# Kernel optimization log

Hardware: AMD Instinct MI355X
Metric: run time of the kernel (lower is better)

Reference implementation:

```python
import jax, jax.numpy as jnp
import numpy as np

N_NODES = 100000
N_EDGES = 1600000
IN_DIM = 128
HID_DIM = 64
OUT_DIM = 128
EPS = 1e-5


def setup_inputs() -> dict:
    key = jax.random.key(0)
    ks = jax.random.split(key, 10)
    feat = jax.random.normal(ks[0], (N_NODES, IN_DIM), dtype=jnp.float32)
    src = jax.random.randint(ks[1], (N_EDGES,), 0, N_NODES)
    dst = jax.random.randint(ks[2], (N_EDGES,), 0, N_NODES)
    # learned params
    gamma = jnp.ones((IN_DIM,), jnp.float32)
    beta = jnp.zeros((IN_DIM,), jnp.float32)
    Wq = jax.random.normal(ks[3], (IN_DIM, HID_DIM), jnp.float32) * 0.05
    bq = jax.random.normal(ks[4], (HID_DIM,), jnp.float32) * 0.05
    Wk = jax.random.normal(ks[5], (IN_DIM, HID_DIM), jnp.float32) * 0.05
    Wv = jax.random.normal(ks[6], (IN_DIM, OUT_DIM), jnp.float32) * 0.05
    We = jax.random.normal(ks[7], (HID_DIM, 1), jnp.float32) * 0.05
    return {"feat": feat, "src": src, "dst": dst, "gamma": gamma, "beta": beta,
            "Wq": Wq, "bq": bq, "Wk": Wk, "Wv": Wv, "We": We}


def reference(feat, src, dst, gamma, beta, Wq, bq, Wk, Wv, We):
    # BatchNorm1d (training-mode batch stats, biased variance)
    mean = jnp.mean(feat, axis=0)
    var = jnp.mean((feat - mean) ** 2, axis=0)
    x = (feat - mean) * jax.lax.rsqrt(var + EPS) * gamma + beta
    # feat_drop = 0.0 -> identity
    q = x @ Wq + bq          # [N, H]
    k = x @ Wk               # [N, H]
    v = x @ Wv               # [N, O]
    # u_add_v: src-node q + dst-node k per edge, then sigmoid and fc_e -> scalar score
    e = jax.nn.sigmoid(q[src] + k[dst]) @ We  # [E, 1]
    e = e[:, 0]                               # [E]
    # edge_softmax: softmax over incoming edges of each destination node
    m = jax.ops.segment_max(e, dst, num_segments=N_NODES)  # [N]
    ex = jnp.exp(e - m[dst])
    s = jax.ops.segment_sum(ex, dst, num_segments=N_NODES)  # [N]
    a = ex / s[dst]                                          # [E]
    # u_mul_e_sum: weighted scatter-sum of source v into destinations
    rst = jax.ops.segment_sum(v[src] * a[:, None], dst, num_segments=N_NODES)  # [N, O]
    return rst
```

## Files before the change

### kernel.cpp

```cpp
#include <hip/hip_runtime.h>
#include <math.h>

#define IN_DIM 128
#define HID 64
#define OUT_DIM 128
#define ELL_W 64
#define FA 512
#define FB 512
constexpr float EPS = 1e-5f;

typedef short short8 __attribute__((ext_vector_type(8)));
typedef float f32x4  __attribute__((ext_vector_type(4)));
typedef int   i32x4  __attribute__((ext_vector_type(4)));


__device__ inline ushort f2bf(float x) {
    __bf16 h = (__bf16)x;
    return *reinterpret_cast<ushort*>(&h);
}
__device__ inline short f2bfs(float x) {
    __bf16 h = (__bf16)x;
    return *reinterpret_cast<short*>(&h);
}
__device__ inline float bf2f(ushort u) {
    union { unsigned u; float f; } c; c.u = ((unsigned)u) << 16;
    return c.f;
}
__device__ inline float4 bf4_to_f4(ushort4 u) {
    return make_float4(bf2f(u.x), bf2f(u.y), bf2f(u.z), bf2f(u.w));
}

__device__ __forceinline__ void fill_edges(
    const int* __restrict__ src, const int* __restrict__ dst,
    int* __restrict__ deg, int* __restrict__ ell,
    int e0, int e1, int bid, int nblk)
{
    int idx    = bid * 256 + threadIdx.x;
    int stride = nblk * 256;
    int nv     = (e1 - e0) >> 2;
    const i32x4* d4p = reinterpret_cast<const i32x4*>(dst + e0);
    const i32x4* s4p = reinterpret_cast<const i32x4*>(src + e0);

    for (int i = idx; i < nv; i += stride) {
        i32x4 d4 = __builtin_nontemporal_load(d4p + i);
        i32x4 s4 = __builtin_nontemporal_load(s4p + i);
        #pragma unroll
        for (int j = 0; j < 4; j++) {
            int d = d4[j];
            int pos = atomicAdd(&deg[d], 1);
            if (pos < ELL_W) ell[(size_t)d * ELL_W + pos] = s4[j];
        }
    }
    for (int e = e0 + (nv << 2) + idx; e < e1; e += stride) {
        int d = dst[e];
        int pos = atomicAdd(&deg[d], 1);
        if (pos < ELL_W) ell[(size_t)d * ELL_W + pos] = src[e];
    }
}

__global__ __launch_bounds__(256) void preA(
    const float* __restrict__ feat, float* __restrict__ ws, int n_nodes,
    const float* __restrict__ Wq, const float* __restrict__ Wk,
    const float* __restrict__ Wv, ushort* __restrict__ Bfrag,
    const int* __restrict__ src, const int* __restrict__ dst,
    int* __restrict__ deg, int* __restrict__ ell, int e1)
{
    int t = threadIdx.x;
    if (blockIdx.x < 256) {
        __shared__ float redS[256], redQ[256];
        int col  = t & 127;
        int half = t >> 7;
        float sum = 0.f, sq = 0.f;
        for (int r = blockIdx.x * 2 + half; r < n_nodes; r += 512) {
            float x = feat[r * IN_DIM + col];
            sum += x; sq += x * x;
        }
        redS[t] = sum; redQ[t] = sq;
        __syncthreads();
        if (t < 128) {
            sum = redS[t] + redS[t + 128];
            sq  = redQ[t] + redQ[t + 128];
            unsafeAtomicAdd(&ws[col], sum);
            unsafeAtomicAdd(&ws[128 + col], sq);
        }
    } else if (blockIdx.x < 256 + 16) {
        int gid  = (blockIdx.x - 256) * 256 + t;
        int f    = gid >> 6;
        int lane = gid & 63;
        int kc = f & 3, ct = (f >> 2) & 3, w = f >> 4;
        int col   = w * 64 + ct * 16 + (lane & 15);
        int kbase = kc * 32 + (lane >> 4) * 8;
        ushort tmp[8];
        #pragma unroll
        for (int j = 0; j < 8; j++) {
            int k = kbase + j;
            float val;
            if (col < 64)       val = Wq[k * HID + col];
            else if (col < 128) val = Wk[k * HID + (col - 64)];
            else                val = Wv[k * OUT_DIM + (col - 128)];
            tmp[j] = f2bf(val);
        }
        ushort* d = &Bfrag[(f * 64 + lane) * 8];
        *(ushort4*)d       = make_ushort4(tmp[0], tmp[1], tmp[2], tmp[3]);
        *(ushort4*)(d + 4) = make_ushort4(tmp[4], tmp[5], tmp[6], tmp[7]);
    } else {
        fill_edges(src, dst, deg, ell, 0, e1, blockIdx.x - 272, FA);
    }
}

__global__ __launch_bounds__(256) void fusedB(
    const float* __restrict__ feat, const ushort* __restrict__ Bfrag,
    const float* __restrict__ bq,
    const float* __restrict__ gamma, const float* __restrict__ beta,
    const float* __restrict__ stats,
    ushort* __restrict__ qvb, ushort* __restrict__ kb, int n_nodes,
    const int* __restrict__ src, const int* __restrict__ dst,
    int* __restrict__ deg, int* __restrict__ ell, int e1, int n_edges,
    int mb)
{
    if (blockIdx.x >= mb) {
        fill_edges(src, dst, deg, ell, e1, n_edges, blockIdx.x - mb, FB);
        return;
    }

    __shared__ float sc[IN_DIM], sh[IN_DIM];
    int tid = threadIdx.x;
    if (tid < 128) {
        float inv_n = 1.0f / (float)n_nodes;
        float mean = stats[tid] * inv_n;
        float var  = stats[128 + tid] * inv_n - mean * mean;
        float s    = gamma[tid] * rsqrtf(var + EPS);
        sc[tid] = s; sh[tid] = beta[tid] - mean * s;
    }

    int w    = tid >> 6;
    int lane = tid & 63;
    int row0 = blockIdx.x * 64;
    int m    = lane & 15;
    int quad = lane >> 4;
    int nm1  = n_nodes - 1;

    short8 bfr[16];
    #pragma unroll
    for (int f = 0; f < 16; f++)
        bfr[f] = *(const short8*)&Bfrag[((w * 16 + f) * 64 + lane) * 8];

    __syncthreads();

    f32x4 acc[4][4] = {};

    #pragma unroll
    for (int kc = 0; kc < 4; kc++) {
        int koff = kc * 32 + quad * 8;
        float4 sc0 = *(const float4*)&sc[koff];
        float4 sc1 = *(const float4*)&sc[koff + 4];
        float4 sh0 = *(const float4*)&sh[koff];
        float4 sh1 = *(const float4*)&sh[koff + 4];
        short8 afr[4];
        #pragma unroll
        for (int rt = 0; rt < 4; rt++) {
            int row = row0 + rt * 16 + m;
            row = row < nm1 ? row : nm1;
            const float* fp = &feat[(size_t)row * IN_DIM + koff];
            float4 x0 = *(const float4*)fp;
            float4 x1 = *(const float4*)(fp + 4);
            afr[rt][0] = f2bfs(x0.x * sc0.x + sh0.x);
            afr[rt][1] = f2bfs(x0.y * sc0.y + sh0.y);
            afr[rt][2] = f2bfs(x0.z * sc0.z + sh0.z);
            afr[rt][3] = f2bfs(x0.w * sc0.w + sh0.w);
            afr[rt][4] = f2bfs(x1.x * sc1.x + sh1.x);
            afr[rt][5] = f2bfs(x1.y * sc1.y + sh1.y);
            afr[rt][6] = f2bfs(x1.z * sc1.z + sh1.z);
            afr[rt][7] = f2bfs(x1.w * sc1.w + sh1.w);
        }
        #pragma unroll
        for (int rt = 0; rt < 4; rt++)
            #pragma unroll
            for (int ct = 0; ct < 4; ct++)
                acc[rt][ct] = __builtin_amdgcn_mfma_f32_16x16x32_bf16(
                    afr[rt], bfr[ct * 4 + kc], acc[rt][ct], 0, 0, 0);
    }

    ushort* base; int ld, cl;
    if (w == 1)      { base = kb;  ld = HID; cl = 0; }
    else             { base = qvb; ld = 192; cl = (w == 0) ? 0 : 64 * (w - 1); }

    #pragma unroll
    for (int ct = 0; ct < 4; ct++) {
        int col = cl + ct * 16 + m;
        float bias = (w == 0) ? bq[ct * 16 + m] : 0.f;
        #pragma unroll
        for (int rt = 0; rt < 4; rt++) {
            int r0 = row0 + rt * 16 + quad * 4;
            #pragma unroll
            for (int r = 0; r < 4; r++)
                base[(size_t)(r0 + r) * ld + col] = f2bf(acc[rt][ct][r] + bias);
        }
    }
}

__global__ __launch_bounds__(256) void gather_ell(
    const int* __restrict__ deg, const int* __restrict__ ell,
    const ushort* __restrict__ qvb, const ushort* __restrict__ kb,
    const float* __restrict__ We,
    float* __restrict__ out, int n_nodes)
{
    int node = (blockIdx.x * 256 + threadIdx.x) >> 6;
    int lane = threadIdx.x & 63;
    if (node >= n_nodes) return;
    int h   = lane & 15;
    int sub = lane >> 4;
    int cnt = deg[node];
    cnt = cnt < ELL_W ? cnt : ELL_W;

    if (cnt == 0) {
        if (sub == 0) {
            float4 z = make_float4(0.f, 0.f, 0.f, 0.f);
            *(float4*)&out[node * OUT_DIM + 4 * h]      = z;
            *(float4*)&out[node * OUT_DIM + 64 + 4 * h] = z;
        }
        return;
    }

    const int* row = &ell[(size_t)node * ELL_W];
    float4 kd = bf4_to_f4(*(const ushort4*)&kb[node * HID + 4 * h]);
    float4 we = *(const float4*)&We[4 * h];
    const float L2E = 1.4426950408889634f;
    we.x *= L2E; we.y *= L2E; we.z *= L2E; we.w *= L2E;

    float4 o0 = make_float4(0.f, 0.f, 0.f, 0.f);
    float4 o1 = make_float4(0.f, 0.f, 0.f, 0.f);
    float ssum = 0.f;

    for (int p0 = 0; p0 < cnt; p0 += 4) {
        int p = p0 + sub;
        bool act = (p < cnt);
        int sN = row[act ? p : 0];
        const ushort* qv = qvb + (size_t)sN * 192;
        float4 qq = bf4_to_f4(*(const ushort4*)(qv + 4 * h));
        float t;
        t  = we.x * __fdividef(1.f, 1.f + __expf(-(qq.x + kd.x)));
        t += we.y * __fdividef(1.f, 1.f + __expf(-(qq.y + kd.y)));
        t += we.z * __fdividef(1.f, 1.f + __expf(-(qq.z + kd.z)));
        t += we.w * __fdividef(1.f, 1.f + __expf(-(qq.w + kd.w)));
        t += __shfl_xor(t, 1);
        t += __shfl_xor(t, 2);
        t += __shfl_xor(t, 4);
        t += __shfl_xor(t, 8);
        float exv = act ? exp2f(t) : 0.f;
        ssum += exv;
        float4 v0 = bf4_to_f4(*(const ushort4*)(qv + 64 + 4 * h));
        float4 v1 = bf4_to_f4(*(const ushort4*)(qv + 128 + 4 * h));
        o0.x += exv * v0.x; o0.y += exv * v0.y;
        o0.z += exv * v0.z; o0.w += exv * v0.w;
        o1.x += exv * v1.x; o1.y += exv * v1.y;
        o1.z += exv * v1.z; o1.w += exv * v1.w;
    }

    ssum += __shfl_xor(ssum, 16); ssum += __shfl_xor(ssum, 32);
    o0.x += __shfl_xor(o0.x, 16); o0.x += __shfl_xor(o0.x, 32);
    o0.y += __shfl_xor(o0.y, 16); o0.y += __shfl_xor(o0.y, 32);
    o0.z += __shfl_xor(o0.z, 16); o0.z += __shfl_xor(o0.z, 32);
    o0.w += __shfl_xor(o0.w, 16); o0.w += __shfl_xor(o0.w, 32);
    o1.x += __shfl_xor(o1.x, 16); o1.x += __shfl_xor(o1.x, 32);
    o1.y += __shfl_xor(o1.y, 16); o1.y += __shfl_xor(o1.y, 32);
    o1.z += __shfl_xor(o1.z, 16); o1.z += __shfl_xor(o1.z, 32);
    o1.w += __shfl_xor(o1.w, 16); o1.w += __shfl_xor(o1.w, 32);

    if (sub == 0) {
        float inv = (ssum > 0.f) ? __fdividef(1.f, ssum) : 0.f;
        o0.x *= inv; o0.y *= inv; o0.z *= inv; o0.w *= inv;
        o1.x *= inv; o1.y *= inv; o1.z *= inv; o1.w *= inv;
        *(float4*)&out[node * OUT_DIM + 4 * h]      = o0;
        *(float4*)&out[node * OUT_DIM + 64 + 4 * h] = o1;
    }
}

extern "C" void kernel_launch(void* const* d_in, const int* in_sizes, int n_in,
                              void* d_out, int out_size, void* d_ws, size_t ws_size,
                              hipStream_t stream)
{
    const float* feat  = (const float*)d_in[0];
    const int*   src   = (const int*)d_in[1];
    const int*   dst   = (const int*)d_in[2];
    const float* gamma = (const float*)d_in[3];
    const float* beta  = (const float*)d_in[4];
    const float* Wq    = (const float*)d_in[5];
    const float* bq    = (const float*)d_in[6];
    const float* Wk    = (const float*)d_in[7];
    const float* Wv    = (const float*)d_in[8];
    const float* We    = (const float*)d_in[9];

    int n_nodes = in_sizes[0] / IN_DIM;
    int n_edges = in_sizes[1];
    int n_pad   = n_nodes + 64;
    int mb      = (n_nodes + 63) / 64;
    int e1      = ((n_edges * 9) / 20) & ~3;

    float* ws = (float*)d_ws;

    int* deg = (int*)(ws + 256);
    int* ell = deg + n_nodes;
    size_t off = 256 + (size_t)n_nodes * (1 + ELL_W);
    off = (off + 3) & ~(size_t)3;
    ushort* qvb   = (ushort*)(ws + off);
    ushort* kb    = qvb + (size_t)n_pad * 192;
    ushort* Bfrag = kb + (size_t)n_pad * HID;

    hipMemsetAsync(ws, 0, (256 + (size_t)n_nodes) * sizeof(float), stream);
    preA<<<256 + 16 + FA, 256, 0, stream>>>(
        feat, ws, n_nodes, Wq, Wk, Wv, Bfrag, src, dst, deg, ell, e1);
    fusedB<<<mb + FB, 256, 0, stream>>>(
        feat, Bfrag, bq, gamma, beta, ws, qvb, kb, n_nodes,
        src, dst, deg, ell, e1, n_edges, mb);
    long long g_threads = (long long)n_nodes * 64;
    gather_ell<<<(int)((g_threads + 255) / 256), 256, 0, stream>>>(
        deg, ell, qvb, kb, We, (float*)d_out, n_nodes);
}
```

Baseline: 409.5 us.

## Fuse all stages into one persistent cooperative kernel with grid syncs

Replaces the memset plus three launches with a single cooperative persistent kernel. It zeroes the workspace, builds the weight fragments, computes BatchNorm stats, fills the ELL adjacency, runs the MFMA projections and does the edge-softmax gather, with grid-wide syncs between phases. This removes launch overhead and the memset. In exchange it serializes edge filling after the stats pass, where before that work overlapped with other stages. It also drops the vectorized nontemporal edge loads and adds grid-sync costs, with persistent loops over nodes replacing a full grid for the gather.

```diff
diff --git a/kernel.cpp b/kernel.cpp
--- a/kernel.cpp
+++ b/kernel.cpp
@@ -1,17 +1,17 @@
 #include <hip/hip_runtime.h>
+#include <hip/hip_cooperative_groups.h>
 #include <math.h>
+
+namespace cg = cooperative_groups;
 
 #define IN_DIM 128
 #define HID 64
 #define OUT_DIM 128
 #define ELL_W 64
-#define FA 512
-#define FB 512
 constexpr float EPS = 1e-5f;
 
 typedef short short8 __attribute__((ext_vector_type(8)));
 typedef float f32x4  __attribute__((ext_vector_type(4)));
-typedef int   i32x4  __attribute__((ext_vector_type(4)));
 
 
 __device__ inline ushort f2bf(float x) {
@@ -30,66 +30,36 @@
     return make_float4(bf2f(u.x), bf2f(u.y), bf2f(u.z), bf2f(u.w));
 }
 
-__device__ __forceinline__ void fill_edges(
+__global__ __launch_bounds__(256, 4) void mega(
+    const float* __restrict__ feat,
     const int* __restrict__ src, const int* __restrict__ dst,
-    int* __restrict__ deg, int* __restrict__ ell,
-    int e0, int e1, int bid, int nblk)
+    const float* __restrict__ gamma, const float* __restrict__ beta,
+    const float* __restrict__ Wq, const float* __restrict__ bq,
+    const float* __restrict__ Wk, const float* __restrict__ Wv,
+    const float* __restrict__ We,
+    float* __restrict__ ws, int* __restrict__ deg, int* __restrict__ ell,
+    ushort* __restrict__ qvb, ushort* __restrict__ kb,
+    ushort* __restrict__ Bfrag, float* __restrict__ out,
+    int n_nodes, int n_edges, int mb)
 {
-    int idx    = bid * 256 + threadIdx.x;
-    int stride = nblk * 256;
-    int nv     = (e1 - e0) >> 2;
-    const i32x4* d4p = reinterpret_cast<const i32x4*>(dst + e0);
-    const i32x4* s4p = reinterpret_cast<const i32x4*>(src + e0);
-
-    for (int i = idx; i < nv; i += stride) {
-        i32x4 d4 = __builtin_nontemporal_load(d4p + i);
-        i32x4 s4 = __builtin_nontemporal_load(s4p + i);
-        #pragma unroll
-        for (int j = 0; j < 4; j++) {
-            int d = d4[j];
-            int pos = atomicAdd(&deg[d], 1);
-            if (pos < ELL_W) ell[(size_t)d * ELL_W + pos] = s4[j];
-        }
-    }
-    for (int e = e0 + (nv << 2) + idx; e < e1; e += stride) {
-        int d = dst[e];
-        int pos = atomicAdd(&deg[d], 1);
-        if (pos < ELL_W) ell[(size_t)d * ELL_W + pos] = src[e];
-    }
-}
-
-__global__ __launch_bounds__(256) void preA(
-    const float* __restrict__ feat, float* __restrict__ ws, int n_nodes,
-    const float* __restrict__ Wq, const float* __restrict__ Wk,
-    const float* __restrict__ Wv, ushort* __restrict__ Bfrag,
-    const int* __restrict__ src, const int* __restrict__ dst,
-    int* __restrict__ deg, int* __restrict__ ell, int e1)
-{
-    int t = threadIdx.x;
-    if (blockIdx.x < 256) {
-        __shared__ float redS[256], redQ[256];
-        int col  = t & 127;
-        int half = t >> 7;
-        float sum = 0.f, sq = 0.f;
-        for (int r = blockIdx.x * 2 + half; r < n_nodes; r += 512) {
-            float x = feat[r * IN_DIM + col];
-            sum += x; sq += x * x;
-        }
-        redS[t] = sum; redQ[t] = sq;
-        __syncthreads();
-        if (t < 128) {
-            sum = redS[t] + redS[t + 128];
-            sq  = redQ[t] + redQ[t + 128];
-            unsafeAtomicAdd(&ws[col], sum);
-            unsafeAtomicAdd(&ws[128 + col], sq);
-        }
-    } else if (blockIdx.x < 256 + 16) {
-        int gid  = (blockIdx.x - 256) * 256 + t;
+    cg::grid_group gg = cg::this_grid();
+    __shared__ float smem[512];
+    int t    = threadIdx.x;
+    int G    = (int)gridDim.x;
+    int gtid = (int)blockIdx.x * 256 + t;
+    int gsz  = G * 256;
+    int w    = t >> 6;
+    int lane = t & 63;
+
+    for (int i = gtid; i < 256; i += gsz) ws[i] = 0.f;
+    for (int i = gtid; i < n_nodes; i += gsz) deg[i] = 0;
+    if (blockIdx.x < 16) {
+        int gid  = (int)blockIdx.x * 256 + t;
         int f    = gid >> 6;
-        int lane = gid & 63;
-        int kc = f & 3, ct = (f >> 2) & 3, w = f >> 4;
-        int col   = w * 64 + ct * 16 + (lane & 15);
-        int kbase = kc * 32 + (lane >> 4) * 8;
+        int l    = gid & 63;
+        int kc = f & 3, ct = (f >> 2) & 3, ww = f >> 4;
+        int col   = ww * 64 + ct * 16 + (l & 15);
+        int kbase = kc * 32 + (l >> 4) * 8;
         ushort tmp[8];
         #pragma unroll
         for (int j = 0; j < 8; j++) {
@@ -100,179 +70,184 @@
             else                val = Wv[k * OUT_DIM + (col - 128)];
             tmp[j] = f2bf(val);
         }
-        ushort* d = &Bfrag[(f * 64 + lane) * 8];
+        ushort* d = &Bfrag[(f * 64 + l) * 8];
         *(ushort4*)d       = make_ushort4(tmp[0], tmp[1], tmp[2], tmp[3]);
         *(ushort4*)(d + 4) = make_ushort4(tmp[4], tmp[5], tmp[6], tmp[7]);
-    } else {
-        fill_edges(src, dst, deg, ell, 0, e1, blockIdx.x - 272, FA);
-    }
-}
-
-__global__ __launch_bounds__(256) void fusedB(
-    const float* __restrict__ feat, const ushort* __restrict__ Bfrag,
-    const float* __restrict__ bq,
-    const float* __restrict__ gamma, const float* __restrict__ beta,
-    const float* __restrict__ stats,
-    ushort* __restrict__ qvb, ushort* __restrict__ kb, int n_nodes,
-    const int* __restrict__ src, const int* __restrict__ dst,
-    int* __restrict__ deg, int* __restrict__ ell, int e1, int n_edges,
-    int mb)
-{
-    if (blockIdx.x >= mb) {
-        fill_edges(src, dst, deg, ell, e1, n_edges, blockIdx.x - mb, FB);
-        return;
-    }
-
-    __shared__ float sc[IN_DIM], sh[IN_DIM];
-    int tid = threadIdx.x;
-    if (tid < 128) {
-        float inv_n = 1.0f / (float)n_nodes;
-        float mean = stats[tid] * inv_n;
-        float var  = stats[128 + tid] * inv_n - mean * mean;
-        float s    = gamma[tid] * rsqrtf(var + EPS);
-        sc[tid] = s; sh[tid] = beta[tid] - mean * s;
-    }
-
-    int w    = tid >> 6;
-    int lane = tid & 63;
-    int row0 = blockIdx.x * 64;
-    int m    = lane & 15;
-    int quad = lane >> 4;
-    int nm1  = n_nodes - 1;
-
-    short8 bfr[16];
-    #pragma unroll
-    for (int f = 0; f < 16; f++)
-        bfr[f] = *(const short8*)&Bfrag[((w * 16 + f) * 64 + lane) * 8];
-
-    __syncthreads();
-
-    f32x4 acc[4][4] = {};
-
-    #pragma unroll
-    for (int kc = 0; kc < 4; kc++) {
-        int koff = kc * 32 + quad * 8;
-        float4 sc0 = *(const float4*)&sc[koff];
-        float4 sc1 = *(const float4*)&sc[koff + 4];
-        float4 sh0 = *(const float4*)&sh[koff];
-        float4 sh1 = *(const float4*)&sh[koff + 4];
-        short8 afr[4];
+    }
+    gg.sync();
+
+    {
+        int col  = t & 127;
+        int half = t >> 7;
+        float sum = 0.f, sq = 0.f;
+        for (int r = (int)blockIdx.x * 2 + half; r < n_nodes; r += G * 2) {
+            float x = feat[r * IN_DIM + col];
+            sum += x; sq += x * x;
+        }
+        smem[t] = sum; smem[256 + t] = sq;
+        __syncthreads();
+        if (t < 128) {
+            sum = smem[t] + smem[t + 128];
+            sq  = smem[256 + t] + smem[256 + t + 128];
+            unsafeAtomicAdd(&ws[t], sum);
+            unsafeAtomicAdd(&ws[128 + t], sq);
+        }
+    }
+    gg.sync();
+
+    for (int e = gtid; e < n_edges; e += gsz) {
+        int d = dst[e];
+        int s = src[e];
+        int pos = atomicAdd(&deg[d], 1);
+        if (pos < ELL_W) ell[(size_t)d * ELL_W + pos] = s;
+    }
+    gg.sync();
+
+    {
+        if (t < 128) {
+            float inv_n = 1.0f / (float)n_nodes;
+            float mean = ws[t] * inv_n;
+            float var  = ws[128 + t] * inv_n - mean * mean;
+            float s    = gamma[t] * rsqrtf(var + EPS);
+            smem[t] = s; smem[128 + t] = beta[t] - mean * s;
+        }
+        int m    = lane & 15;
+        int quad = lane >> 4;
+        int nm1  = n_nodes - 1;
+        short8 bfr[16];
         #pragma unroll
-        for (int rt = 0; rt < 4; rt++) {
-            int row = row0 + rt * 16 + m;
-            row = row < nm1 ? row : nm1;
-            const float* fp = &feat[(size_t)row * IN_DIM + koff];
-            float4 x0 = *(const float4*)fp;
-            float4 x1 = *(const float4*)(fp + 4);
-            afr[rt][0] = f2bfs(x0.x * sc0.x + sh0.x);
-            afr[rt][1] = f2bfs(x0.y * sc0.y + sh0.y);
-            afr[rt][2] = f2bfs(x0.z * sc0.z + sh0.z);
-            afr[rt][3] = f2bfs(x0.w * sc0.w + sh0.w);
-            afr[rt][4] = f2bfs(x1.x * sc1.x + sh1.x);
-            afr[rt][5] = f2bfs(x1.y * sc1.y + sh1.y);
-            afr[rt][6] = f2bfs(x1.z * sc1.z + sh1.z);
-            afr[rt][7] = f2bfs(x1.w * sc1.w + sh1.w);
-        }
-        #pragma unroll
-        for (int rt = 0; rt < 4; rt++)
+        for (int f = 0; f < 16; f++)
+            bfr[f] = *(const short8*)&Bfrag[((w * 16 + f) * 64 + lane) * 8];
+        __syncthreads();
+        const float* sc = smem;
+        const float* sh = smem + 128;
+
+        for (int mi = (int)blockIdx.x; mi < mb; mi += G) {
+            int row0 = mi * 64;
+            f32x4 acc[4][4] = {};
             #pragma unroll
-            for (int ct = 0; ct < 4; ct++)
-                acc[rt][ct] = __builtin_amdgcn_mfma_f32_16x16x32_bf16(
-                    afr[rt], bfr[ct * 4 + kc], acc[rt][ct], 0, 0, 0);
-    }
-
-    ushort* base; int ld, cl;
-    if (w == 1)      { base = kb;  ld = HID; cl = 0; }
-    else             { base = qvb; ld = 192; cl = (w == 0) ? 0 : 64 * (w - 1); }
-
-    #pragma unroll
-    for (int ct = 0; ct < 4; ct++) {
-        int col = cl + ct * 16 + m;
-        float bias = (w == 0) ? bq[ct * 16 + m] : 0.f;
-        #pragma unroll
-        for (int rt = 0; rt < 4; rt++) {
-            int r0 = row0 + rt * 16 + quad * 4;
+            for (int kc = 0; kc < 4; kc++) {
+                int koff = kc * 32 + quad * 8;
+                float4 sc0 = *(const float4*)&sc[koff];
+                float4 sc1 = *(const float4*)&sc[koff + 4];
+                float4 sh0 = *(const float4*)&sh[koff];
+                float4 sh1 = *(const float4*)&sh[koff + 4];
+                short8 afr[4];
+                #pragma unroll
+                for (int rt = 0; rt < 4; rt++) {
+                    int row = row0 + rt * 16 + m;
+                    row = row < nm1 ? row : nm1;
+                    const float* fp = &feat[(size_t)row * IN_DIM + koff];
+                    float4 x0 = *(const float4*)fp;
+                    float4 x1 = *(const float4*)(fp + 4);
+                    afr[rt][0] = f2bfs(x0.x * sc0.x + sh0.x);
+                    afr[rt][1] = f2bfs(x0.y * sc0.y + sh0.y);
+                    afr[rt][2] = f2bfs(x0.z * sc0.z + sh0.z);
+                    afr[rt][3] = f2bfs(x0.w * sc0.w + sh0.w);
+                    afr[rt][4] = f2bfs(x1.x * sc1.x + sh1.x);
+                    afr[rt][5] = f2bfs(x1.y * sc1.y + sh1.y);
+                    afr[rt][6] = f2bfs(x1.z * sc1.z + sh1.z);
+                    afr[rt][7] = f2bfs(x1.w * sc1.w + sh1.w);
+                }
+                #pragma unroll
+                for (int rt = 0; rt < 4; rt++)
+                    #pragma unroll
+                    for (int ct = 0; ct < 4; ct++)
+                        acc[rt][ct] = __builtin_amdgcn_mfma_f32_16x16x32_bf16(
+                            afr[rt], bfr[ct * 4 + kc], acc[rt][ct], 0, 0, 0);
+            }
+
+            ushort* base; int ld, cl;
+            if (w == 1)      { base = kb;  ld = HID; cl = 0; }
+            else             { base = qvb; ld = 192; cl = (w == 0) ? 0 : 64 * (w - 1); }
+
             #pragma unroll
-            for (int r = 0; r < 4; r++)
-                base[(size_t)(r0 + r) * ld + col] = f2bf(acc[rt][ct][r] + bias);
-        }
-    }
-}
-
-__global__ __launch_bounds__(256) void gather_ell(
-    const int* __restrict__ deg, const int* __restrict__ ell,
-    const ushort* __restrict__ qvb, const ushort* __restrict__ kb,
-    const float* __restrict__ We,
-    float* __restrict__ out, int n_nodes)
-{
-    int node = (blockIdx.x * 256 + threadIdx.x) >> 6;
-    int lane = threadIdx.x & 63;
-    if (node >= n_nodes) return;
-    int h   = lane & 15;
-    int sub = lane >> 4;
-    int cnt = deg[node];
-    cnt = cnt < ELL_W ? cnt : ELL_W;
-
-    if (cnt == 0) {
-        if (sub == 0) {
-            float4 z = make_float4(0.f, 0.f, 0.f, 0.f);
-            *(float4*)&out[node * OUT_DIM + 4 * h]      = z;
-            *(float4*)&out[node * OUT_DIM + 64 + 4 * h] = z;
-        }
-        return;
-    }
-
-    const int* row = &ell[(size_t)node * ELL_W];
-    float4 kd = bf4_to_f4(*(const ushort4*)&kb[node * HID + 4 * h]);
-    float4 we = *(const float4*)&We[4 * h];
-    const float L2E = 1.4426950408889634f;
-    we.x *= L2E; we.y *= L2E; we.z *= L2E; we.w *= L2E;
-
-    float4 o0 = make_float4(0.f, 0.f, 0.f, 0.f);
-    float4 o1 = make_float4(0.f, 0.f, 0.f, 0.f);
-    float ssum = 0.f;
-
-    for (int p0 = 0; p0 < cnt; p0 += 4) {
-        int p = p0 + sub;
-        bool act = (p < cnt);
-        int sN = row[act ? p : 0];
-        const ushort* qv = qvb + (size_t)sN * 192;
-        float4 qq = bf4_to_f4(*(const ushort4*)(qv + 4 * h));
-        float t;
-        t  = we.x * __fdividef(1.f, 1.f + __expf(-(qq.x + kd.x)));
-        t += we.y * __fdividef(1.f, 1.f + __expf(-(qq.y + kd.y)));
-        t += we.z * __fdividef(1.f, 1.f + __expf(-(qq.z + kd.z)));
-        t += we.w * __fdividef(1.f, 1.f + __expf(-(qq.w + kd.w)));
-        t += __shfl_xor(t, 1);
-        t += __shfl_xor(t, 2);
-        t += __shfl_xor(t, 4);
-        t += __shfl_xor(t, 8);
-        float exv = act ? exp2f(t) : 0.f;
-        ssum += exv;
-        float4 v0 = bf4_to_f4(*(const ushort4*)(qv + 64 + 4 * h));
-        float4 v1 = bf4_to_f4(*(const ushort4*)(qv + 128 + 4 * h));
-        o0.x += exv * v0.x; o0.y += exv * v0.y;
-        o0.z += exv * v0.z; o0.w += exv * v0.w;
-        o1.x += exv * v1.x; o1.y += exv * v1.y;
-        o1.z += exv * v1.z; o1.w += exv * v1.w;
-    }
-
-    ssum += __shfl_xor(ssum, 16); ssum += __shfl_xor(ssum, 32);
-    o0.x += __shfl_xor(o0.x, 16); o0.x += __shfl_xor(o0.x, 32);
-    o0.y += __shfl_xor(o0.y, 16); o0.y += __shfl_xor(o0.y, 32);
-    o0.z += __shfl_xor(o0.z, 16); o0.z += __shfl_xor(o0.z, 32);
-    o0.w += __shfl_xor(o0.w, 16); o0.w += __shfl_xor(o0.w, 32);
-    o1.x += __shfl_xor(o1.x, 16); o1.x += __shfl_xor(o1.x, 32);
-    o1.y += __shfl_xor(o1.y, 16); o1.y += __shfl_xor(o1.y, 32);
-    o1.z += __shfl_xor(o1.z, 16); o1.z += __shfl_xor(o1.z, 32);
-    o1.w += __shfl_xor(o1.w, 16); o1.w += __shfl_xor(o1.w, 32);
-
-    if (sub == 0) {
-        float inv = (ssum > 0.f) ? __fdividef(1.f, ssum) : 0.f;
-        o0.x *= inv; o0.y *= inv; o0.z *= inv; o0.w *= inv;
-        o1.x *= inv; o1.y *= inv; o1.z *= inv; o1.w *= inv;
-        *(float4*)&out[node * OUT_DIM + 4 * h]      = o0;
-        *(float4*)&out[node * OUT_DIM + 64 + 4 * h] = o1;
+            for (int ct = 0; ct < 4; ct++) {
+                int col = cl + ct * 16 + m;
+                float bias = (w == 0) ? bq[ct * 16 + m] : 0.f;
+                #pragma unroll
+                for (int rt = 0; rt < 4; rt++) {
+                    int r0 = row0 + rt * 16 + quad * 4;
+                    #pragma unroll
+                    for (int r = 0; r < 4; r++)
+                        base[(size_t)(r0 + r) * ld + col] = f2bf(acc[rt][ct][r] + bias);
+                }
+            }
+        }
+    }
+    gg.sync();
+
+    {
+        int h   = lane & 15;
+        int sub = lane >> 4;
+        float4 we = *(const float4*)&We[4 * h];
+        const float L2E = 1.4426950408889634f;
+        we.x *= L2E; we.y *= L2E; we.z *= L2E; we.w *= L2E;
+
+        for (int node = (int)blockIdx.x * 4 + w; node < n_nodes; node += G * 4) {
+            int cnt = deg[node];
+            cnt = cnt < ELL_W ? cnt : ELL_W;
+            int ob = node * OUT_DIM + 4 * h;
+
+            if (cnt == 0) {
+                if (sub == 0) {
+                    float4 z = make_float4(0.f, 0.f, 0.f, 0.f);
+                    *(float4*)&out[ob]      = z;
+                    *(float4*)&out[ob + 64] = z;
+                }
+                continue;
+            }
+
+            const int* row = &ell[(size_t)node * ELL_W];
+            float4 kd = bf4_to_f4(*(const ushort4*)&kb[node * HID + 4 * h]);
+
+            float4 o0 = make_float4(0.f, 0.f, 0.f, 0.f);
+            float4 o1 = make_float4(0.f, 0.f, 0.f, 0.f);
+            float ssum = 0.f;
+
+            for (int p0 = 0; p0 < cnt; p0 += 4) {
+                int p = p0 + sub;
+                bool act = (p < cnt);
+                int sN = row[act ? p : 0];
+                const ushort* qv = qvb + (size_t)sN * 192;
+                float4 qq = bf4_to_f4(*(const ushort4*)(qv + 4 * h));
+                float tt;
+                tt  = we.x * __fdividef(1.f, 1.f + __expf(-(qq.x + kd.x)));
+                tt += we.y * __fdividef(1.f, 1.f + __expf(-(qq.y + kd.y)));
+                tt += we.z * __fdividef(1.f, 1.f + __expf(-(qq.z + kd.z)));
+                tt += we.w * __fdividef(1.f, 1.f + __expf(-(qq.w + kd.w)));
+                tt += __shfl_xor(tt, 1);
+                tt += __shfl_xor(tt, 2);
+                tt += __shfl_xor(tt, 4);
+                tt += __shfl_xor(tt, 8);
+                float exv = act ? exp2f(tt) : 0.f;
+                ssum += exv;
+                float4 v0 = bf4_to_f4(*(const ushort4*)(qv + 64 + 4 * h));
+                float4 v1 = bf4_to_f4(*(const ushort4*)(qv + 128 + 4 * h));
+                o0.x += exv * v0.x; o0.y += exv * v0.y;
+                o0.z += exv * v0.z; o0.w += exv * v0.w;
+                o1.x += exv * v1.x; o1.y += exv * v1.y;
+                o1.z += exv * v1.z; o1.w += exv * v1.w;
+            }
+
+            ssum += __shfl_xor(ssum, 16); ssum += __shfl_xor(ssum, 32);
+            o0.x += __shfl_xor(o0.x, 16); o0.x += __shfl_xor(o0.x, 32);
+            o0.y += __shfl_xor(o0.y, 16); o0.y += __shfl_xor(o0.y, 32);
+            o0.z += __shfl_xor(o0.z, 16); o0.z += __shfl_xor(o0.z, 32);
+            o0.w += __shfl_xor(o0.w, 16); o0.w += __shfl_xor(o0.w, 32);
+            o1.x += __shfl_xor(o1.x, 16); o1.x += __shfl_xor(o1.x, 32);
+            o1.y += __shfl_xor(o1.y, 16); o1.y += __shfl_xor(o1.y, 32);
+            o1.z += __shfl_xor(o1.z, 16); o1.z += __shfl_xor(o1.z, 32);
+            o1.w += __shfl_xor(o1.w, 16); o1.w += __shfl_xor(o1.w, 32);
+
+            if (sub == 0) {
+                float inv = (ssum > 0.f) ? __fdividef(1.f, ssum) : 0.f;
+                o0.x *= inv; o0.y *= inv; o0.z *= inv; o0.w *= inv;
+                o1.x *= inv; o1.y *= inv; o1.z *= inv; o1.w *= inv;
+                *(float4*)&out[ob]      = o0;
+                *(float4*)&out[ob + 64] = o1;
+            }
+        }
     }
 }
 
@@ -295,7 +270,6 @@
     int n_edges = in_sizes[1];
     int n_pad   = n_nodes + 64;
     int mb      = (n_nodes + 63) / 64;
-    int e1      = ((n_edges * 9) / 20) & ~3;
 
     float* ws = (float*)d_ws;
 
@@ -306,14 +280,32 @@
     ushort* qvb   = (ushort*)(ws + off);
     ushort* kb    = qvb + (size_t)n_pad * 192;
     ushort* Bfrag = kb + (size_t)n_pad * HID;
-
-    hipMemsetAsync(ws, 0, (256 + (size_t)n_nodes) * sizeof(float), stream);
-    preA<<<256 + 16 + FA, 256, 0, stream>>>(
-        feat, ws, n_nodes, Wq, Wk, Wv, Bfrag, src, dst, deg, ell, e1);
-    fusedB<<<mb + FB, 256, 0, stream>>>(
-        feat, Bfrag, bq, gamma, beta, ws, qvb, kb, n_nodes,
-        src, dst, deg, ell, e1, n_edges, mb);
-    long long g_threads = (long long)n_nodes * 64;
-    gather_ell<<<(int)((g_threads + 255) / 256), 256, 0, stream>>>(
-        deg, ell, qvb, kb, We, (float*)d_out, n_nodes);
-}
+    float*  outp  = (float*)d_out;
+
+    static int s_grid = 0;
+    if (s_grid == 0) {
+        int maxB = 0;
+        (void)hipOccupancyMaxActiveBlocksPerMultiprocessor(
+            &maxB, reinterpret_cast<const void*>(mega), 256, 0);
+        if (maxB < 1) maxB = 1;
+        if (maxB > 8) maxB = 8;
+        hipDeviceProp_t prop;
+        int dev = 0;
+        (void)hipGetDevice(&dev);
+        int ncu = 256;
+        if (hipGetDeviceProperties(&prop, dev) == hipSuccess &&
+            prop.multiProcessorCount > 0)
+            ncu = prop.multiProcessorCount;
+        s_grid = ncu * maxB;
+    }
+
+    void* args[] = {
+        (void*)&feat, (void*)&src, (void*)&dst, (void*)&gamma, (void*)&beta,
+        (void*)&Wq, (void*)&bq, (void*)&Wk, (void*)&Wv, (void*)&We,
+        (void*)&ws, (void*)&deg, (void*)&ell, (void*)&qvb, (void*)&kb,
+        (void*)&Bfrag, (void*)&outp, (void*)&n_nodes, (void*)&n_edges,
+        (void*)&mb
+    };
+    (void)hipLaunchCooperativeKernel(reinterpret_cast<void*>(mega),
+                                     dim3(s_grid), dim3(256), args, 0, stream);
+}
```

After: 804.0 us. +96.4%, slower.

## Split ELL build into partitioned kernel and prescale q/k by log2e

Applied to the files above, without the earlier changes.

Moves the edge-to-ELL fill out of the preprocessing and MFMA kernels into a separate kernel. Each block handles one of 8 destination-node partitions, so atomics and ELL writes from a given block stay within a smaller address range, at the cost of every block reading the full edge list. The q and k projections are now stored pre-multiplied by log2(e), which lets the gather kernel use exp2f instead of __expf in the sigmoid. The separate launches also remove the overlap of edge filling with the BN-stats and MFMA work.

```diff
diff --git a/kernel.cpp b/kernel.cpp
--- a/kernel.cpp
+++ b/kernel.cpp
@@ -5,8 +5,7 @@
 #define HID 64
 #define OUT_DIM 128
 #define ELL_W 64
-#define FA 512
-#define FB 512
+#define NPART 8
 constexpr float EPS = 1e-5f;
 
 typedef short short8 __attribute__((ext_vector_type(8)));
@@ -30,40 +29,10 @@
     return make_float4(bf2f(u.x), bf2f(u.y), bf2f(u.z), bf2f(u.w));
 }
 
-__device__ __forceinline__ void fill_edges(
-    const int* __restrict__ src, const int* __restrict__ dst,
-    int* __restrict__ deg, int* __restrict__ ell,
-    int e0, int e1, int bid, int nblk)
-{
-    int idx    = bid * 256 + threadIdx.x;
-    int stride = nblk * 256;
-    int nv     = (e1 - e0) >> 2;
-    const i32x4* d4p = reinterpret_cast<const i32x4*>(dst + e0);
-    const i32x4* s4p = reinterpret_cast<const i32x4*>(src + e0);
-
-    for (int i = idx; i < nv; i += stride) {
-        i32x4 d4 = __builtin_nontemporal_load(d4p + i);
-        i32x4 s4 = __builtin_nontemporal_load(s4p + i);
-        #pragma unroll
-        for (int j = 0; j < 4; j++) {
-            int d = d4[j];
-            int pos = atomicAdd(&deg[d], 1);
-            if (pos < ELL_W) ell[(size_t)d * ELL_W + pos] = s4[j];
-        }
-    }
-    for (int e = e0 + (nv << 2) + idx; e < e1; e += stride) {
-        int d = dst[e];
-        int pos = atomicAdd(&deg[d], 1);
-        if (pos < ELL_W) ell[(size_t)d * ELL_W + pos] = src[e];
-    }
-}
-
-__global__ __launch_bounds__(256) void preA(
+__global__ __launch_bounds__(256) void pre(
     const float* __restrict__ feat, float* __restrict__ ws, int n_nodes,
     const float* __restrict__ Wq, const float* __restrict__ Wk,
-    const float* __restrict__ Wv, ushort* __restrict__ Bfrag,
-    const int* __restrict__ src, const int* __restrict__ dst,
-    int* __restrict__ deg, int* __restrict__ ell, int e1)
+    const float* __restrict__ Wv, ushort* __restrict__ Bfrag)
 {
     int t = threadIdx.x;
     if (blockIdx.x < 256) {
@@ -83,7 +52,7 @@
             unsafeAtomicAdd(&ws[col], sum);
             unsafeAtomicAdd(&ws[128 + col], sq);
         }
-    } else if (blockIdx.x < 256 + 16) {
+    } else {
         int gid  = (blockIdx.x - 256) * 256 + t;
         int f    = gid >> 6;
         int lane = gid & 63;
@@ -103,26 +72,56 @@
         ushort* d = &Bfrag[(f * 64 + lane) * 8];
         *(ushort4*)d       = make_ushort4(tmp[0], tmp[1], tmp[2], tmp[3]);
         *(ushort4*)(d + 4) = make_ushort4(tmp[4], tmp[5], tmp[6], tmp[7]);
-    } else {
-        fill_edges(src, dst, deg, ell, 0, e1, blockIdx.x - 272, FA);
-    }
-}
-
-__global__ __launch_bounds__(256) void fusedB(
+    }
+}
+
+__global__ __launch_bounds__(256) void fill_ell_part(
+    const int* __restrict__ src, const int* __restrict__ dst,
+    int* __restrict__ deg, int* __restrict__ ell,
+    int n_edges, int part_size)
+{
+    int p  = blockIdx.x & (NPART - 1);
+    int gb = blockIdx.x >> 3;
+    int nb = gridDim.x >> 3;
+    unsigned lo = (unsigned)(p * part_size);
+    unsigned ps = (unsigned)part_size;
+
+    int idx    = gb * 256 + threadIdx.x;
+    int stride = nb * 256;
+    int n4     = n_edges >> 2;
+
+    const i32x4* dst4 = reinterpret_cast<const i32x4*>(dst);
+    const i32x4* src4 = reinterpret_cast<const i32x4*>(src);
+
+    for (int i = idx; i < n4; i += stride) {
+        i32x4 d4 = __builtin_nontemporal_load(dst4 + i);
+        i32x4 s4 = __builtin_nontemporal_load(src4 + i);
+        #pragma unroll
+        for (int j = 0; j < 4; j++) {
+            unsigned d = (unsigned)d4[j];
+            if (d - lo < ps) {
+                int pos = atomicAdd(&deg[d], 1);
+                if (pos < ELL_W) ell[(size_t)d * ELL_W + pos] = s4[j];
+            }
+        }
+    }
+    for (int e = (n4 << 2) + idx; e < n_edges; e += stride) {
+        unsigned d = (unsigned)dst[e];
+        if (d - lo < ps) {
+            int pos = atomicAdd(&deg[d], 1);
+            if (pos < ELL_W) ell[(size_t)d * ELL_W + pos] = src[e];
+        }
+    }
+}
+
+__global__ __launch_bounds__(256) void mfma_qkv(
     const float* __restrict__ feat, const ushort* __restrict__ Bfrag,
     const float* __restrict__ bq,
     const float* __restrict__ gamma, const float* __restrict__ beta,
     const float* __restrict__ stats,
-    ushort* __restrict__ qvb, ushort* __restrict__ kb, int n_nodes,
-    const int* __restrict__ src, const int* __restrict__ dst,
-    int* __restrict__ deg, int* __restrict__ ell, int e1, int n_edges,
-    int mb)
-{
-    if (blockIdx.x >= mb) {
-        fill_edges(src, dst, deg, ell, e1, n_edges, blockIdx.x - mb, FB);
-        return;
-    }
-
+    ushort* __restrict__ qvb, ushort* __restrict__ kb,
+    int n_nodes)
+{
     __shared__ float sc[IN_DIM], sh[IN_DIM];
     int tid = threadIdx.x;
     if (tid < 128) {
@@ -181,7 +180,9 @@
                     afr[rt], bfr[ct * 4 + kc], acc[rt][ct], 0, 0, 0);
     }
 
+    const float L2E = 1.4426950408889634f;
     ushort* base; int ld, cl;
+    float scale = (w <= 1) ? L2E : 1.f;
     if (w == 1)      { base = kb;  ld = HID; cl = 0; }
     else             { base = qvb; ld = 192; cl = (w == 0) ? 0 : 64 * (w - 1); }
 
@@ -194,7 +195,8 @@
             int r0 = row0 + rt * 16 + quad * 4;
             #pragma unroll
             for (int r = 0; r < 4; r++)
-                base[(size_t)(r0 + r) * ld + col] = f2bf(acc[rt][ct][r] + bias);
+                base[(size_t)(r0 + r) * ld + col] =
+                    f2bf((acc[rt][ct][r] + bias) * scale);
         }
     }
 }
@@ -239,10 +241,10 @@
         const ushort* qv = qvb + (size_t)sN * 192;
         float4 qq = bf4_to_f4(*(const ushort4*)(qv + 4 * h));
         float t;
-        t  = we.x * __fdividef(1.f, 1.f + __expf(-(qq.x + kd.x)));
-        t += we.y * __fdividef(1.f, 1.f + __expf(-(qq.y + kd.y)));
-        t += we.z * __fdividef(1.f, 1.f + __expf(-(qq.z + kd.z)));
-        t += we.w * __fdividef(1.f, 1.f + __expf(-(qq.w + kd.w)));
+        t  = we.x * __fdividef(1.f, 1.f + exp2f(-(qq.x + kd.x)));
+        t += we.y * __fdividef(1.f, 1.f + exp2f(-(qq.y + kd.y)));
+        t += we.z * __fdividef(1.f, 1.f + exp2f(-(qq.z + kd.z)));
+        t += we.w * __fdividef(1.f, 1.f + exp2f(-(qq.w + kd.w)));
         t += __shfl_xor(t, 1);
         t += __shfl_xor(t, 2);
         t += __shfl_xor(t, 4);
@@ -294,8 +296,7 @@
     int n_nodes = in_sizes[0] / IN_DIM;
     int n_edges = in_sizes[1];
     int n_pad   = n_nodes + 64;
-    int mb      = (n_nodes + 63) / 64;
-    int e1      = ((n_edges * 9) / 20) & ~3;
+    int part_size = (n_nodes + NPART - 1) / NPART;
 
     float* ws = (float*)d_ws;
 
@@ -308,11 +309,11 @@
     ushort* Bfrag = kb + (size_t)n_pad * HID;
 
     hipMemsetAsync(ws, 0, (256 + (size_t)n_nodes) * sizeof(float), stream);
-    preA<<<256 + 16 + FA, 256, 0, stream>>>(
-        feat, ws, n_nodes, Wq, Wk, Wv, Bfrag, src, dst, deg, ell, e1);
-    fusedB<<<mb + FB, 256, 0, stream>>>(
-        feat, Bfrag, bq, gamma, beta, ws, qvb, kb, n_nodes,
-        src, dst, deg, ell, e1, n_edges, mb);
+    pre<<<272, 256, 0, stream>>>(feat, ws, n_nodes, Wq, Wk, Wv, Bfrag);
+    fill_ell_part<<<2048, 256, 0, stream>>>(
+        src, dst, deg, ell, n_edges, part_size);
+    mfma_qkv<<<(n_nodes + 63) / 64, 256, 0, stream>>>(
+        feat, Bfrag, bq, gamma, beta, ws, qvb, kb, n_nodes);
     long long g_threads = (long long)n_nodes * 64;
     gather_ell<<<(int)((g_threads + 255) / 256), 256, 0, stream>>>(
         deg, ell, qvb, kb, We, (float*)d_out, n_nodes);
```

After: 412.7 us. Within noise of the previous version (+0.8%).
